# Optimization experiments

Measured on AMD Instinct MI355X. Metric: run time of the kernel, lower is better.

The kernel has to match this reference:

```python
import jax, jax.numpy as jnp
import numpy as np


def _linear_init(key, fan_in, fan_out):
    k1, k2 = jax.random.split(key)
    sc = 1.0 / np.sqrt(fan_in)
    w = jax.random.uniform(k1, (fan_in, fan_out), jnp.float32, -sc, sc)
    b = jax.random.uniform(k2, (fan_out,), jnp.float32, -sc, sc)
    return w, b


def setup_inputs() -> dict:
    key = jax.random.key(0)
    ks = jax.random.split(key, 16)
    b, s, q, c, d = 8, 5, 15, 256, 4
    inp = {
        'support_xf': jax.random.normal(ks[0], (b, s, c, d, d), jnp.float32),
        'query_xf': jax.random.normal(ks[1], (b, q, c, d, d), jnp.float32),
        'support_y': jax.random.randint(ks[2], (b, s), 0, 5),
        'query_y': jax.random.randint(ks[3], (b, q), 0, 5),
    }
    g_dims = [(516, 256), (256, 256), (256, 256), (256, 256)]
    for i, (fi, fo) in enumerate(g_dims):
        w, bb = _linear_init(ks[4 + i], fi, fo)
        inp['g_w%d' % (i + 1)] = w
        inp['g_b%d' % (i + 1)] = bb
    f_dims = [(256, 256), (256, 256), (256, 29), (29, 1)]
    for i, (fi, fo) in enumerate(f_dims):
        w, bb = _linear_init(ks[8 + i], fi, fo)
        inp['f_w%d' % (i + 1)] = w
        inp['f_b%d' % (i + 1)] = bb
    return inp


def reference(support_xf, query_xf, support_y, query_y,
              g_w1, g_b1, g_w2, g_b2, g_w3, g_b3, g_w4, g_b4,
              f_w1, f_b1, f_w2, f_b2, f_w3, f_b3, f_w4, f_b4):
    b, s, c, d, _ = support_xf.shape
    q = query_xf.shape[1]
    d2 = d * d
    relu = jax.nn.relu
    # coord channels: ch0 = i/d (row), ch1 = j/d (col), shape [2, d, d]
    ii = jnp.arange(d, dtype=support_xf.dtype) / d
    coord = jnp.stack([jnp.broadcast_to(ii[:, None], (d, d)),
                       jnp.broadcast_to(ii[None, :], (d, d))], axis=0)
    sup = jnp.concatenate([support_xf, jnp.broadcast_to(coord, (b, s, 2, d, d))], axis=2)
    qry = jnp.concatenate([query_xf, jnp.broadcast_to(coord, (b, q, 2, d, d))], axis=2)
    cp = c + 2
    sup = sup.reshape(b, s, cp, d2).transpose(0, 1, 3, 2)  # [b,s,d2,cp]
    qry = qry.reshape(b, q, cp, d2).transpose(0, 1, 3, 2)  # [b,q,d2,cp]
    # pair[b,q,s,m,n] = concat(support feature at spatial n, query feature at spatial m)
    sup_e = jnp.broadcast_to(sup[:, None, :, None, :, :], (b, q, s, d2, d2, cp))
    qry_e = jnp.broadcast_to(qry[:, :, None, :, None, :], (b, q, s, d2, d2, cp))
    x = jnp.concatenate([sup_e, qry_e], axis=-1)  # [b,q,s,d2,d2,2*cp]
    # g MLP applied per pair
    x = relu(x @ g_w1 + g_b1)
    x = relu(x @ g_w2 + g_b2)
    x = relu(x @ g_w3 + g_b3)
    x = relu(x @ g_w4 + g_b4)
    xf = x.sum(axis=(3, 4))  # sum over d^4 pairs -> [b,q,s,256]
    # f MLP (Dropout is identity in eval mode)
    y = relu(xf @ f_w1 + f_b1)
    y = relu(y @ f_w2 + f_b2)
    y = relu(y @ f_w3 + f_b3)
    score = jax.nn.sigmoid(y @ f_w4 + f_b4)[..., 0]  # [b,q,s]
    label = (support_y[:, None, :] == query_y[:, :, None]).astype(score.dtype)
    loss = jnp.sum((label - score) ** 2) / b
    return loss
```

## Files before the change

### kernel.cpp

```cpp
#include <hip/hip_runtime.h>

typedef __attribute__((ext_vector_type(8))) __bf16 bf16x8;
typedef __attribute__((ext_vector_type(8))) short short8;
typedef __attribute__((ext_vector_type(4))) float f32x4;
typedef unsigned int u32;

static __device__ __forceinline__ unsigned short f2bf(float f) {
    u32 u = __float_as_uint(f);
    u += 0x7FFFu + ((u >> 16) & 1u);
    return (unsigned short)(u >> 16);
}
static __device__ __forceinline__ u32 cvt_pk_bf16(float lo, float hi) {
    u32 r;
    asm("v_cvt_pk_bf16_f32 %0, %1, %2" : "=v"(r) : "v"(lo), "v"(hi));
    return r;
}
static __device__ __forceinline__ bf16x8 as_bf16x8(short8 v) {
    return __builtin_bit_cast(bf16x8, v);
}
static __device__ __forceinline__ f32x4 mfma16(short8 a, short8 b, f32x4 c) {
    return __builtin_amdgcn_mfma_f32_16x16x32_bf16(as_bf16x8(a), as_bf16x8(b), c, 0, 0, 0);
}

#define NB 8
#define NS 5
#define NQ 15
#define A_OFF_F 0
#define B_OFF_F (640*256)
#define XF_OFF_F (B_OFF_F + 1920*256)
#define WF_OFF_BYTES ((XF_OFF_F + 600*1024)*4)
#define WF1_OFF_BYTES (WF_OFF_BYTES + 48*8192)
#define WFF_OFF_BYTES (WF1_OFF_BYTES + 32*9216)
#define WF3_OFF_BYTES (WFF_OFF_BYTES + 32*8192)

__global__ void kA(const float* __restrict__ w1, unsigned short* __restrict__ wf1) {
    int c1 = blockIdx.x;
    int l = threadIdx.x;
    int S = c1 >> 4, tt = c1 & 15;
    int nn = tt * 16 + (l & 15);
    for (int kk = 0; kk < 9; ++kk) {
        int k0 = kk * 32 + (l >> 4) * 8;
        short8 ov;
        #pragma unroll
        for (int j = 0; j < 8; ++j) {
            int kb = k0 + j;
            float v = (kb < 258) ? w1[(size_t)(S * 258 + kb) * 256 + nn] : 0.0f;
            ov[j] = (short)f2bf(v);
        }
        *(short8*)((char*)wf1 + (size_t)c1 * 9216 + kk * 1024 + l * 16) = ov;
    }
}

__global__ void kB(const float* __restrict__ sup, const float* __restrict__ qry,
                   const unsigned short* __restrict__ wf1, const float* __restrict__ gb1,
                   const float* __restrict__ w2, const float* __restrict__ w3,
                   const float* __restrict__ w4,
                   const float* __restrict__ fw1, const float* __restrict__ fw2,
                   const float* __restrict__ fw3,
                   float* __restrict__ ws, unsigned short* __restrict__ wf,
                   unsigned short* __restrict__ wff, unsigned short* __restrict__ wf3,
                   float* __restrict__ out) {
    __shared__ short Xf[4608];
    int bid = blockIdx.x;
    int t = threadIdx.x;
    int w = t >> 6, l = t & 63;
    int g = l >> 4, c = l & 15;

    if (bid >= 160) {
        if (bid < 172) {
            int cid = (bid - 160) * 4 + w;
            int L = cid >> 4, tt = cid & 15;
            const float* W = (L == 0) ? w2 : ((L == 1) ? w3 : w4);
            int nn = tt * 16 + (l & 15);
            #pragma unroll
            for (int kk = 0; kk < 8; ++kk) {
                int k0 = kk * 32 + (l >> 4) * 8;
                short8 ov;
                #pragma unroll
                for (int j = 0; j < 8; ++j)
                    ov[j] = (short)f2bf(W[(size_t)(k0 + j) * 256 + nn]);
                *(short8*)((char*)wf + (size_t)cid * 8192 + kk * 1024 + l * 16) = ov;
            }
        } else if (bid == 172) {
            if (w < 2) {
                int tt = w;
                int nn = tt * 16 + (l & 15);
                #pragma unroll
                for (int kk = 0; kk < 8; ++kk) {
                    int k0 = kk * 32 + (l >> 4) * 8;
                    short8 ov;
                    #pragma unroll
                    for (int j = 0; j < 8; ++j) {
                        float v = (nn < 29) ? fw3[(size_t)(k0 + j) * 29 + nn] : 0.0f;
                        ov[j] = (short)f2bf(v);
                    }
                    *(short8*)((char*)wf3 + (size_t)tt * 8192 + kk * 1024 + l * 16) = ov;
                }
            } else if (w == 2 && l == 0) {
                out[0] = 0.0f;
            }
        } else {
            int cid = (bid - 173) * 4 + w;
            int Lf = cid >> 4, tt = cid & 15;
            const float* W = (Lf == 0) ? fw1 : fw2;
            int nn = tt * 16 + (l & 15);
            #pragma unroll
            for (int kk = 0; kk < 8; ++kk) {
                int k0 = kk * 32 + (l >> 4) * 8;
                short8 ov;
                #pragma unroll
                for (int j = 0; j < 8; ++j)
                    ov[j] = (short)f2bf(W[(size_t)(k0 + j) * 256 + nn]);
                *(short8*)((char*)wff + (size_t)cid * 8192 + kk * 1024 + l * 16) = ov;
            }
        }
        return;
    }

    bool isA = (bid < 40);
    int S = isA ? 0 : 1;
    int cell = isA ? bid : (bid - 40);
    const float* src = (isA ? sup : qry) + (size_t)cell * 4096;
    float* dst0 = ws + (isA ? A_OFF_F : B_OFF_F);
    char* Xb = (char*)Xf;

    for (int kk = w; kk < 9; kk += 4) {
        int kbase = kk * 32 + g * 8;
        float v[8];
        #pragma unroll
        for (int j = 0; j < 8; ++j) {
            int kb = kbase + j;
            float x;
            if (kb < 256)       x = src[(size_t)kb * 16 + c];
            else if (kb == 256) x = (float)(c >> 2) * 0.25f;
            else if (kb == 257) x = (float)(c & 3) * 0.25f;
            else                x = 0.0f;
            v[j] = x;
        }
        uint4 hv;
        hv.x = cvt_pk_bf16(v[0], v[1]);
        hv.y = cvt_pk_bf16(v[2], v[3]);
        hv.z = cvt_pk_bf16(v[4], v[5]);
        hv.w = cvt_pk_bf16(v[6], v[7]);
        *(uint4*)(Xb + (size_t)kk * 1024 + l * 16) = hv;
    }
    __syncthreads();

    const char* wbase = (const char*)wf1 + (size_t)(S * 16 + w * 4) * 9216;
    short8 wcur[4];
    #pragma unroll
    for (int tti = 0; tti < 4; ++tti)
        wcur[tti] = *(const short8*)(wbase + (size_t)tti * 9216 + l * 16);

    f32x4 acc[4];
    #pragma unroll
    for (int tti = 0; tti < 4; ++tti) acc[tti] = (f32x4){0.f, 0.f, 0.f, 0.f};

    #pragma unroll
    for (int kk = 0; kk < 9; ++kk) {
        int kn = kk + 1; if (kn > 8) kn = 8;
        short8 wnxt[4];
        #pragma unroll
        for (int tti = 0; tti < 4; ++tti)
            wnxt[tti] = *(const short8*)(wbase + (size_t)tti * 9216 + kn * 1024 + l * 16);
        short8 h = *(const short8*)(Xb + (size_t)kk * 1024 + l * 16);
        #pragma unroll
        for (int tti = 0; tti < 4; ++tti)
            acc[tti] = mfma16(wcur[tti], h, acc[tti]);
        #pragma unroll
        for (int tti = 0; tti < 4; ++tti) wcur[tti] = wnxt[tti];
    }

    #pragma unroll
    for (int tti = 0; tti < 4; ++tti) {
        int col0 = w * 64 + tti * 16 + g * 4;
        float4 bv = {0.f, 0.f, 0.f, 0.f};
        if (S == 0) bv = *(const float4*)(gb1 + col0);
        int row = cell * 16 + c;
        float4 o;
        o.x = acc[tti][0] + bv.x;
        o.y = acc[tti][1] + bv.y;
        o.z = acc[tti][2] + bv.z;
        o.w = acc[tti][3] + bv.w;
        *(float4*)(dst0 + (size_t)row * 256 + col0) = o;
    }
}

__launch_bounds__(512, 4)
__global__ void k3_g(const float* __restrict__ wsA, const float* __restrict__ wsB,
                     const unsigned short* __restrict__ wf,
                     const float* __restrict__ gb2, const float* __restrict__ gb3,
                     const float* __restrict__ gb4, float* __restrict__ xf) {
    __shared__ short Hf[32768];
    __shared__ float bs[768];
    int bid = blockIdx.x;
    int bqs = bid >> 1, half = bid & 1;
    int b = bqs / 75, rem = bqs % 75, qi = rem / 5, si = rem % 5;
    int t = threadIdx.x;
    int w = t >> 6, l = t & 63;
    int g = l >> 4, c = l & 15;
    int wp = w >> 2, wn = w & 3;
    char* Hb = (char*)Hf;
    const char* wfb = (const char*)wf;

    if (t < 256) { bs[t] = gb2[t]; bs[256 + t] = gb3[t]; bs[512 + t] = gb4[t]; }

    short8 wcur[4];
    #pragma unroll
    for (int tti = 0; tti < 4; ++tti)
        wcur[tti] = *(const short8*)(wfb + (size_t)(wn * 4 + tti) * 8192 + l * 16);

    {
        const float* Arow = wsA + (size_t)(b * NS + si) * 4096 + c * 256;
        const float* Brow = wsB + (size_t)(b * NQ + qi) * 4096 + (half * 8 + w) * 256;
        #pragma unroll
        for (int kk = 0; kk < 8; ++kk) {
            const float* ap = Arow + kk * 32 + g * 8;
            const float* bp = Brow + kk * 32 + g * 8;
            float4 a0 = *(const float4*)ap, a1 = *(const float4*)(ap + 4);
            float4 b0 = *(const float4*)bp, b1 = *(const float4*)(bp + 4);
            uint4 hv;
            hv.x = cvt_pk_bf16(fmaxf(a0.x + b0.x, 0.f), fmaxf(a0.y + b0.y, 0.f));
            hv.y = cvt_pk_bf16(fmaxf(a0.z + b0.z, 0.f), fmaxf(a0.w + b0.w, 0.f));
            hv.z = cvt_pk_bf16(fmaxf(a1.x + b1.x, 0.f), fmaxf(a1.y + b1.y, 0.f));
            hv.w = cvt_pk_bf16(fmaxf(a1.z + b1.z, 0.f), fmaxf(a1.w + b1.w, 0.f));
            *(uint4*)(Hb + (size_t)(w * 8 + kk) * 1024 + l * 16) = hv;
        }
    }
    __syncthreads();

    #pragma unroll 1
    for (int L = 0; L < 3; ++L) {
        f32x4 acc[4][4];
        #pragma unroll
        for (int pg = 0; pg < 4; ++pg)
            #pragma unroll
            for (int tti = 0; tti < 4; ++tti)
                acc[pg][tti] = (f32x4){0.f, 0.f, 0.f, 0.f};

        #pragma unroll
        for (int kk = 0; kk < 8; ++kk) {
            int s = L * 8 + kk + 1; if (s > 23) s = 23;
            int Ln = s >> 3, kn = s & 7;
            short8 wnxt[4];
            #pragma unroll
            for (int tti = 0; tti < 4; ++tti)
                wnxt[tti] = *(const short8*)(wfb +
                    (size_t)(Ln * 16 + wn * 4 + tti) * 8192 + kn * 1024 + l * 16);
            #pragma unroll
            for (int pg = 0; pg < 4; ++pg) {
                short8 h = *(const short8*)(Hb +
                    (size_t)((wp * 4 + pg) * 8 + kk) * 1024 + l * 16);
                #pragma unroll
                for (int tti = 0; tti < 4; ++tti)
                    acc[pg][tti] = mfma16(wcur[tti], h, acc[pg][tti]);
            }
            #pragma unroll
            for (int tti = 0; tti < 4; ++tti) wcur[tti] = wnxt[tti];
        }

        float4 bv[4];
        #pragma unroll
        for (int tti = 0; tti < 4; ++tti)
            bv[tti] = *(const float4*)(bs + L * 256 + wn * 64 + tti * 16 + g * 4);

        if (L < 2) {
            __syncthreads();
            #pragma unroll
            for (int pg = 0; pg < 4; ++pg) {
                int m = wp * 4 + pg;
                #pragma unroll
                for (int tti = 0; tti < 4; ++tti) {
                    uint2 q;
                    q.x = cvt_pk_bf16(fmaxf(acc[pg][tti][0] + bv[tti].x, 0.f),
                                      fmaxf(acc[pg][tti][1] + bv[tti].y, 0.f));
                    q.y = cvt_pk_bf16(fmaxf(acc[pg][tti][2] + bv[tti].z, 0.f),
                                      fmaxf(acc[pg][tti][3] + bv[tti].w, 0.f));
                    int kk2 = wn * 2 + (tti >> 1);
                    int dlane = ((tti & 1) * 2 + (g >> 1)) * 16 + c;
                    *(uint2*)(Hb + (size_t)(m * 8 + kk2) * 1024 + dlane * 16 + (g & 1) * 8) = q;
                }
            }
            __syncthreads();
        } else {
            #pragma unroll
            for (int tti = 0; tti < 4; ++tti) {
                float s0 = 0.f, s1 = 0.f, s2 = 0.f, s3 = 0.f;
                #pragma unroll
                for (int pg = 0; pg < 4; ++pg) {
                    s0 += fmaxf(acc[pg][tti][0] + bv[tti].x, 0.f);
                    s1 += fmaxf(acc[pg][tti][1] + bv[tti].y, 0.f);
                    s2 += fmaxf(acc[pg][tti][2] + bv[tti].z, 0.f);
                    s3 += fmaxf(acc[pg][tti][3] + bv[tti].w, 0.f);
                }
                #pragma unroll
                for (int d = 1; d < 16; d <<= 1) {
                    s0 += __shfl_xor(s0, d); s1 += __shfl_xor(s1, d);
                    s2 += __shfl_xor(s2, d); s3 += __shfl_xor(s3, d);
                }
                if (c == 0) {
                    float4 o = {s0, s1, s2, s3};
                    *(float4*)(xf + (((size_t)bqs * 2 + half) * 2 + wp) * 256 +
                               wn * 64 + tti * 16 + g * 4) = o;
                }
            }
        }
    }
}

__launch_bounds__(512, 1)
__global__ void k4_f(const float* __restrict__ xf,
                     const unsigned short* __restrict__ wff,
                     const unsigned short* __restrict__ wf3,
                     const float* __restrict__ fb1, const float* __restrict__ fb2,
                     const float* __restrict__ fb3,
                     const float* __restrict__ fw4, const float* __restrict__ fb4,
                     const int* __restrict__ sy, const int* __restrict__ qy,
                     float* __restrict__ out) {
    __shared__ short Hf[16384];
    __shared__ float bs[512];
    __shared__ float bs3[32];
    __shared__ float y3[64][32];
    int bid = blockIdx.x;
    int t = threadIdx.x;
    int w = t >> 6, l = t & 63;
    int g = l >> 4, c = l & 15;
    char* Hb = (char*)Hf;
    const char* wfb = (const char*)wff;

    bs[t & 511] = (t < 256) ? fb1[t] : fb2[t - 256];
    if (t < 32) bs3[t] = (t < 29) ? fb3[t] : 0.0f;

    for (int fi = w; fi < 32; fi += 8) {
        int m = fi >> 3, kk = fi & 7;
        int row = bid * 64 + m * 16 + c;
        if (row > 599) row = 599;
        const float* xr = xf + (size_t)row * 1024;
        int kb = kk * 32 + g * 8;
        float v[8];
        #pragma unroll
        for (int j = 0; j < 8; ++j) {
            int f = kb + j;
            v[j] = xr[f] + xr[256 + f] + xr[512 + f] + xr[768 + f];
        }
        uint4 hv;
        hv.x = cvt_pk_bf16(v[0], v[1]);
        hv.y = cvt_pk_bf16(v[2], v[3]);
        hv.z = cvt_pk_bf16(v[4], v[5]);
        hv.w = cvt_pk_bf16(v[6], v[7]);
        *(uint4*)(Hb + (size_t)(m * 8 + kk) * 1024 + l * 16) = hv;
    }
    __syncthreads();

    int wp = w >> 2, wn = w & 3;
    short8 wcur[4];
    #pragma unroll
    for (int tti = 0; tti < 4; ++tti)
        wcur[tti] = *(const short8*)(wfb + (size_t)(wn * 4 + tti) * 8192 + l * 16);

    #pragma unroll 1
    for (int L = 0; L < 2; ++L) {
        f32x4 acc[2][4];
        #pragma unroll
        for (int pg = 0; pg < 2; ++pg)
            #pragma unroll
            for (int tti = 0; tti < 4; ++tti)
                acc[pg][tti] = (f32x4){0.f, 0.f, 0.f, 0.f};

        #pragma unroll
        for (int kk = 0; kk < 8; ++kk) {
            int s = L * 8 + kk + 1; if (s > 15) s = 15;
            int Ln = s >> 3, kn = s & 7;
            short8 wnxt[4];
            #pragma unroll
            for (int tti = 0; tti < 4; ++tti)
                wnxt[tti] = *(const short8*)(wfb +
                    (size_t)(Ln * 16 + wn * 4 + tti) * 8192 + kn * 1024 + l * 16);
            #pragma unroll
            for (int pg = 0; pg < 2; ++pg) {
                short8 h = *(const short8*)(Hb +
                    (size_t)((wp * 2 + pg) * 8 + kk) * 1024 + l * 16);
                #pragma unroll
                for (int tti = 0; tti < 4; ++tti)
                    acc[pg][tti] = mfma16(wcur[tti], h, acc[pg][tti]);
            }
            #pragma unroll
            for (int tti = 0; tti < 4; ++tti) wcur[tti] = wnxt[tti];
        }

        float4 bv[4];
        #pragma unroll
        for (int tti = 0; tti < 4; ++tti)
            bv[tti] = *(const float4*)(bs + L * 256 + wn * 64 + tti * 16 + g * 4);

        __syncthreads();
        #pragma unroll
        for (int pg = 0; pg < 2; ++pg) {
            int m = wp * 2 + pg;
            #pragma unroll
            for (int tti = 0; tti < 4; ++tti) {
                uint2 q;
                q.x = cvt_pk_bf16(fmaxf(acc[pg][tti][0] + bv[tti].x, 0.f),
                                  fmaxf(acc[pg][tti][1] + bv[tti].y, 0.f));
                q.y = cvt_pk_bf16(fmaxf(acc[pg][tti][2] + bv[tti].z, 0.f),
                                  fmaxf(acc[pg][tti][3] + bv[tti].w, 0.f));
                int kk2 = wn * 2 + (tti >> 1);
                int dlane = ((tti & 1) * 2 + (g >> 1)) * 16 + c;
                *(uint2*)(Hb + (size_t)(m * 8 + kk2) * 1024 + dlane * 16 + (g & 1) * 8) = q;
            }
        }
        __syncthreads();
    }

    {
        int m = w >> 1, tt = w & 1;
        f32x4 a3 = {0.f, 0.f, 0.f, 0.f};
        #pragma unroll
        for (int kk = 0; kk < 8; ++kk) {
            short8 wv = *(const short8*)((const char*)wf3 +
                (size_t)(tt * 8 + kk) * 1024 + l * 16);
            short8 h = *(const short8*)(Hb + (size_t)(m * 8 + kk) * 1024 + l * 16);
            a3 = mfma16(wv, h, a3);
        }
        #pragma unroll
        for (int r = 0; r < 4; ++r) {
            int oc = tt * 16 + g * 4 + r;
            float v = a3[r] + bs3[oc];
            y3[m * 16 + c][oc] = v > 0.f ? v : 0.f;
        }
    }
    __syncthreads();

    if (t < 64) {
        int bqs = bid * 64 + t;
        if (bqs < 600) {
            float z = fb4[0];
            #pragma unroll
            for (int k = 0; k < 29; ++k) z += y3[t][k] * fw4[k];
            float score = 1.0f / (1.0f + __expf(-z));
            int b = bqs / 75, rem = bqs % 75, qi = rem / 5, si = rem % 5;
            float label = (sy[b * NS + si] == qy[b * NQ + qi]) ? 1.0f : 0.0f;
            float d = label - score;
            atomicAdd(out, d * d * 0.125f);
        }
    }
}

extern "C" void kernel_launch(void* const* d_in, const int* in_sizes, int n_in,
                              void* d_out, int out_size, void* d_ws, size_t ws_size,
                              hipStream_t stream) {
    const float* sup = (const float*)d_in[0];
    const float* qry = (const float*)d_in[1];
    const int*   sy  = (const int*)d_in[2];
    const int*   qy  = (const int*)d_in[3];
    const float* gw1 = (const float*)d_in[4];
    const float* gb1 = (const float*)d_in[5];
    const float* gw2 = (const float*)d_in[6];
    const float* gb2 = (const float*)d_in[7];
    const float* gw3 = (const float*)d_in[8];
    const float* gb3 = (const float*)d_in[9];
    const float* gw4 = (const float*)d_in[10];
    const float* gb4 = (const float*)d_in[11];
    const float* fw1 = (const float*)d_in[12];
    const float* fb1 = (const float*)d_in[13];
    const float* fw2 = (const float*)d_in[14];
    const float* fb2 = (const float*)d_in[15];
    const float* fw3 = (const float*)d_in[16];
    const float* fb3 = (const float*)d_in[17];
    const float* fw4 = (const float*)d_in[18];
    const float* fb4 = (const float*)d_in[19];

    float* ws = (float*)d_ws;
    float* A  = ws + A_OFF_F;
    float* B  = ws + B_OFF_F;
    float* xf = ws + XF_OFF_F;
    unsigned short* wf  = (unsigned short*)((char*)d_ws + WF_OFF_BYTES);
    unsigned short* wf1 = (unsigned short*)((char*)d_ws + WF1_OFF_BYTES);
    unsigned short* wff = (unsigned short*)((char*)d_ws + WFF_OFF_BYTES);
    unsigned short* wf3 = (unsigned short*)((char*)d_ws + WF3_OFF_BYTES);
    float* out = (float*)d_out;

    kA<<<32, 64, 0, stream>>>(gw1, wf1);
    kB<<<181, 256, 0, stream>>>(sup, qry, wf1, gb1, gw2, gw3, gw4,
                                fw1, fw2, fw3, ws, wf, wff, wf3, out);
    k3_g<<<1200, 512, 0, stream>>>(A, B, wf, gb2, gb3, gb4, xf);
    k4_f<<<10, 512, 0, stream>>>(xf, wff, wf3, fb1, fb2, fb3, fw4, fb4, sy, qy, out);
}
```

Before: 111.7 us.

## Split g-MLP blocks into quarters and stage weights via async global-to-LDS loads

Measured after the change: 122.3 us. 9.5% more time.

```diff
diff --git a/kernel.cpp b/kernel.cpp
--- a/kernel.cpp
+++ b/kernel.cpp
@@ -186,33 +186,41 @@
     }
 }
 
-__launch_bounds__(512, 4)
+__launch_bounds__(256, 2)
 __global__ void k3_g(const float* __restrict__ wsA, const float* __restrict__ wsB,
                      const unsigned short* __restrict__ wf,
                      const float* __restrict__ gb2, const float* __restrict__ gb3,
                      const float* __restrict__ gb4, float* __restrict__ xf) {
-    __shared__ short Hf[32768];
-    __shared__ float bs[768];
+    __shared__ short Hf[16384];
+    __shared__ short Wl[24576];
     int bid = blockIdx.x;
-    int bqs = bid >> 1, half = bid & 1;
+    int bqs = bid >> 2, quarter = bid & 3;
     int b = bqs / 75, rem = bqs % 75, qi = rem / 5, si = rem % 5;
     int t = threadIdx.x;
     int w = t >> 6, l = t & 63;
     int g = l >> 4, c = l & 15;
-    int wp = w >> 2, wn = w & 3;
     char* Hb = (char*)Hf;
+    char* Wb = (char*)Wl;
     const char* wfb = (const char*)wf;
 
-    if (t < 256) { bs[t] = gb2[t]; bs[256 + t] = gb3[t]; bs[512 + t] = gb4[t]; }
-
-    short8 wcur[4];
-    #pragma unroll
-    for (int tti = 0; tti < 4; ++tti)
-        wcur[tti] = *(const short8*)(wfb + (size_t)(wn * 4 + tti) * 8192 + l * 16);
+    auto stage = [&](int s) {
+        const char* src = wfb + (size_t)((s >> 3) * 16 + w * 4) * 8192
+                              + (size_t)(s & 7) * 1024 + (size_t)l * 16;
+        char* dst = Wb + (s % 3) * 16384 + w * 4096;
+        #pragma unroll
+        for (int i = 0; i < 4; ++i)
+            __builtin_amdgcn_global_load_lds(
+                (const __attribute__((address_space(1))) unsigned int*)(src + i * 8192),
+                (__attribute__((address_space(3))) unsigned int*)(dst + i * 1024),
+                16, 0, 0);
+    };
+
+    stage(0);
+    stage(1);
 
     {
         const float* Arow = wsA + (size_t)(b * NS + si) * 4096 + c * 256;
-        const float* Brow = wsB + (size_t)(b * NQ + qi) * 4096 + (half * 8 + w) * 256;
+        const float* Brow = wsB + (size_t)(b * NQ + qi) * 4096 + (quarter * 4 + w) * 256;
         #pragma unroll
         for (int kk = 0; kk < 8; ++kk) {
             const float* ap = Arow + kk * 32 + g * 8;
@@ -229,79 +237,97 @@
     }
     __syncthreads();
 
-    #pragma unroll 1
-    for (int L = 0; L < 3; ++L) {
-        f32x4 acc[4][4];
+    float4 bv[4];
+    #pragma unroll
+    for (int tti = 0; tti < 4; ++tti)
+        bv[tti] = *(const float4*)(gb2 + w * 64 + tti * 16 + g * 4);
+
+    f32x4 acc[4][4];
+    #pragma unroll
+    for (int pg = 0; pg < 4; ++pg)
+        #pragma unroll
+        for (int tti = 0; tti < 4; ++tti)
+            acc[pg][tti] = (f32x4){0.f, 0.f, 0.f, 0.f};
+
+    #pragma unroll
+    for (int s = 0; s < 24; ++s) {
+        const int L = s >> 3, kk = s & 7;
+        if (s == 23) {
+            asm volatile("s_waitcnt vmcnt(0)" ::: "memory");
+        } else if (s > 0) {
+            asm volatile("s_waitcnt vmcnt(4)" ::: "memory");
+        }
+        if (kk == 0 && L == 1) {
+            #pragma unroll
+            for (int tti = 0; tti < 4; ++tti)
+                bv[tti] = *(const float4*)(gb3 + w * 64 + tti * 16 + g * 4);
+        }
+        if (kk == 0 && L == 2) {
+            #pragma unroll
+            for (int tti = 0; tti < 4; ++tti)
+                bv[tti] = *(const float4*)(gb4 + w * 64 + tti * 16 + g * 4);
+        }
+        if (s + 2 < 24) stage(s + 2);
+
+        short8 Wr[4], Hr[4];
+        #pragma unroll
+        for (int i = 0; i < 4; ++i)
+            Wr[i] = *(const short8*)(Wb + (s % 3) * 16384 + (w * 4 + i) * 1024 + l * 16);
         #pragma unroll
         for (int pg = 0; pg < 4; ++pg)
+            Hr[pg] = *(const short8*)(Hb + (size_t)(pg * 8 + kk) * 1024 + l * 16);
+        #pragma unroll
+        for (int pg = 0; pg < 4; ++pg)
             #pragma unroll
             for (int tti = 0; tti < 4; ++tti)
-                acc[pg][tti] = (f32x4){0.f, 0.f, 0.f, 0.f};
-
-        #pragma unroll
-        for (int kk = 0; kk < 8; ++kk) {
-            int s = L * 8 + kk + 1; if (s > 23) s = 23;
-            int Ln = s >> 3, kn = s & 7;
-            short8 wnxt[4];
-            #pragma unroll
-            for (int tti = 0; tti < 4; ++tti)
-                wnxt[tti] = *(const short8*)(wfb +
-                    (size_t)(Ln * 16 + wn * 4 + tti) * 8192 + kn * 1024 + l * 16);
-            #pragma unroll
-            for (int pg = 0; pg < 4; ++pg) {
-                short8 h = *(const short8*)(Hb +
-                    (size_t)((wp * 4 + pg) * 8 + kk) * 1024 + l * 16);
-                #pragma unroll
-                for (int tti = 0; tti < 4; ++tti)
-                    acc[pg][tti] = mfma16(wcur[tti], h, acc[pg][tti]);
-            }
-            #pragma unroll
-            for (int tti = 0; tti < 4; ++tti) wcur[tti] = wnxt[tti];
-        }
-
-        float4 bv[4];
-        #pragma unroll
-        for (int tti = 0; tti < 4; ++tti)
-            bv[tti] = *(const float4*)(bs + L * 256 + wn * 64 + tti * 16 + g * 4);
-
-        if (L < 2) {
-            __syncthreads();
-            #pragma unroll
-            for (int pg = 0; pg < 4; ++pg) {
-                int m = wp * 4 + pg;
+                acc[pg][tti] = mfma16(Wr[tti], Hr[pg], acc[pg][tti]);
+
+        if (kk == 7) {
+            if (L < 2) {
+                __builtin_amdgcn_s_barrier();
+                #pragma unroll
+                for (int pg = 0; pg < 4; ++pg) {
+                    #pragma unroll
+                    for (int tti = 0; tti < 4; ++tti) {
+                        uint2 q;
+                        q.x = cvt_pk_bf16(fmaxf(acc[pg][tti][0] + bv[tti].x, 0.f),
+                                          fmaxf(acc[pg][tti][1] + bv[tti].y, 0.f));
+                        q.y = cvt_pk_bf16(fmaxf(acc[pg][tti][2] + bv[tti].z, 0.f),
+                                          fmaxf(acc[pg][tti][3] + bv[tti].w, 0.f));
+                        int kk2 = w * 2 + (tti >> 1);
+                        int dlane = ((tti & 1) * 2 + (g >> 1)) * 16 + c;
+                        *(uint2*)(Hb + (size_t)(pg * 8 + kk2) * 1024 +
+                                  dlane * 16 + (g & 1) * 8) = q;
+                    }
+                }
+                asm volatile("s_waitcnt lgkmcnt(0)" ::: "memory");
+                __builtin_amdgcn_s_barrier();
+                #pragma unroll
+                for (int pg = 0; pg < 4; ++pg)
+                    #pragma unroll
+                    for (int tti = 0; tti < 4; ++tti)
+                        acc[pg][tti] = (f32x4){0.f, 0.f, 0.f, 0.f};
+            } else {
                 #pragma unroll
                 for (int tti = 0; tti < 4; ++tti) {
-                    uint2 q;
-                    q.x = cvt_pk_bf16(fmaxf(acc[pg][tti][0] + bv[tti].x, 0.f),
-                                      fmaxf(acc[pg][tti][1] + bv[tti].y, 0.f));
-                    q.y = cvt_pk_bf16(fmaxf(acc[pg][tti][2] + bv[tti].z, 0.f),
-                                      fmaxf(acc[pg][tti][3] + bv[tti].w, 0.f));
-                    int kk2 = wn * 2 + (tti >> 1);
-                    int dlane = ((tti & 1) * 2 + (g >> 1)) * 16 + c;
-                    *(uint2*)(Hb + (size_t)(m * 8 + kk2) * 1024 + dlane * 16 + (g & 1) * 8) = q;
-                }
-            }
-            __syncthreads();
-        } else {
-            #pragma unroll
-            for (int tti = 0; tti < 4; ++tti) {
-                float s0 = 0.f, s1 = 0.f, s2 = 0.f, s3 = 0.f;
-                #pragma unroll
-                for (int pg = 0; pg < 4; ++pg) {
-                    s0 += fmaxf(acc[pg][tti][0] + bv[tti].x, 0.f);
-                    s1 += fmaxf(acc[pg][tti][1] + bv[tti].y, 0.f);
-                    s2 += fmaxf(acc[pg][tti][2] + bv[tti].z, 0.f);
-                    s3 += fmaxf(acc[pg][tti][3] + bv[tti].w, 0.f);
-                }
-                #pragma unroll
-                for (int d = 1; d < 16; d <<= 1) {
-                    s0 += __shfl_xor(s0, d); s1 += __shfl_xor(s1, d);
-                    s2 += __shfl_xor(s2, d); s3 += __shfl_xor(s3, d);
-                }
-                if (c == 0) {
-                    float4 o = {s0, s1, s2, s3};
-                    *(float4*)(xf + (((size_t)bqs * 2 + half) * 2 + wp) * 256 +
-                               wn * 64 + tti * 16 + g * 4) = o;
+                    float s0 = 0.f, s1 = 0.f, s2 = 0.f, s3 = 0.f;
+                    #pragma unroll
+                    for (int pg = 0; pg < 4; ++pg) {
+                        s0 += fmaxf(acc[pg][tti][0] + bv[tti].x, 0.f);
+                        s1 += fmaxf(acc[pg][tti][1] + bv[tti].y, 0.f);
+                        s2 += fmaxf(acc[pg][tti][2] + bv[tti].z, 0.f);
+                        s3 += fmaxf(acc[pg][tti][3] + bv[tti].w, 0.f);
+                    }
+                    #pragma unroll
+                    for (int d = 1; d < 16; d <<= 1) {
+                        s0 += __shfl_xor(s0, d); s1 += __shfl_xor(s1, d);
+                        s2 += __shfl_xor(s2, d); s3 += __shfl_xor(s3, d);
+                    }
+                    if (c == 0) {
+                        float4 o = {s0, s1, s2, s3};
+                        *(float4*)(xf + ((size_t)bqs * 4 + quarter) * 256 +
+                                   w * 64 + tti * 16 + g * 4) = o;
+                    }
                 }
             }
         }
@@ -483,6 +509,6 @@
     kA<<<32, 64, 0, stream>>>(gw1, wf1);
     kB<<<181, 256, 0, stream>>>(sup, qry, wf1, gb1, gw2, gw3, gw4,
                                 fw1, fw2, fw3, ws, wf, wff, wf3, out);
-    k3_g<<<1200, 512, 0, stream>>>(A, B, wf, gb2, gb3, gb4, xf);
+    k3_g<<<2400, 256, 0, stream>>>(A, B, wf, gb2, gb3, gb4, xf);
     k4_f<<<10, 512, 0, stream>>>(xf, wff, wf3, fb1, fb2, fb3, fw4, fb4, sy, qy, out);
 }
```
